# Kernel tuning notes

Measured on AMD Instinct MI355X. Metric: run time of the kernel, lower is better.

Reference implementation:

```python
import jax, jax.numpy as jnp
import numpy as np

B, IN, S, PD, P, D = 8192, 19000, 256, 128, 16, 64  # batch, input_dim, shared_dim, pathway_dim, n_pathways, n_drugs


def setup_inputs() -> dict:
    key = jax.random.key(0)
    ks = jax.random.split(key, 6)
    x = jax.random.normal(ks[0], (B, IN), dtype=jnp.float32)
    drug_indices = jax.random.randint(ks[1], (B,), 0, D, dtype=jnp.int32)
    W1 = jax.random.normal(ks[2], (IN, S), dtype=jnp.float32) / np.float32(np.sqrt(IN))
    b1 = jnp.zeros((S,), jnp.float32)
    Wp = jax.random.normal(ks[3], (P, S, PD), dtype=jnp.float32) / np.float32(np.sqrt(S))
    bp = jnp.zeros((P, PD), jnp.float32)
    Wd = jax.random.normal(ks[4], (D, PD), dtype=jnp.float32) / np.float32(np.sqrt(PD))
    bd = jnp.zeros((D,), jnp.float32)
    drug_to_pw = (jnp.arange(D, dtype=jnp.int32) % P)  # drug -> pathway routing table (i%16 per init_kwargs)
    return dict(x=x, drug_indices=drug_indices, W1=W1, b1=b1, Wp=Wp, bp=bp, Wd=Wd, bd=bd, drug_to_pw=drug_to_pw)


def reference(x, drug_indices, W1, b1, Wp, bp, Wd, bd, drug_to_pw):
    # shared encoder (dropout is identity in eval)
    h = jax.nn.relu(x @ W1 + b1)                                  # [B, S]
    # run all pathway experts densely (P is small), then per-sample select
    all_pw = jax.nn.relu(jnp.einsum('bs,psd->bpd', h, Wp) + bp)   # [B, P, PD]
    pw_idx = drug_to_pw[drug_indices]                             # [B]
    pw_out = jnp.take_along_axis(all_pw, pw_idx[:, None, None], axis=1)[:, 0]  # [B, PD]
    # per-sample drug head: gather row of Wd and dot
    out = jnp.sum(pw_out * Wd[drug_indices], axis=-1) + bd[drug_indices]       # [B]
    return out
```

## Files before the change

### kernel.cpp

```cpp
#include <hip/hip_runtime.h>

#define KREAL 19000
#define KP    19008
#define NSTEPS 594
#define BM 128
#define BN 256
#define MBLK 64
#define BATCH 8192
#define SDIM 256
#define PDIM 128

typedef __attribute__((ext_vector_type(8))) short frag_ab;
typedef __attribute__((ext_vector_type(4))) float frag_cd;

static __device__ __forceinline__ short f2bf(float f) {
    union { float f; unsigned u; } cv; cv.f = f;
    unsigned u = cv.u;
    u += 0x7fffu + ((u >> 16) & 1u);
    return (short)(u >> 16);
}

static __device__ __forceinline__ short4 cvt4(float4 v) {
    short4 p;
    p.x = f2bf(v.x); p.y = f2bf(v.y); p.z = f2bf(v.z); p.w = f2bf(v.w);
    return p;
}

__global__ void transpose_w1(const float* __restrict__ W1, short* __restrict__ W1t) {
    __shared__ float tile[32][33];
    int k0 = blockIdx.x * 32;
    int n0 = blockIdx.y * 32;
    int tx = threadIdx.x & 31;
    int ty = threadIdx.x >> 5;
#pragma unroll
    for (int i = 0; i < 32; i += 8) {
        int k = k0 + ty + i;
        tile[ty + i][tx] = (k < KREAL) ? W1[(long)k * SDIM + n0 + tx] : 0.f;
    }
    __syncthreads();
#pragma unroll
    for (int i = 0; i < 32; i += 8) {
        int n = n0 + ty + i;
        W1t[(long)n * KP + k0 + tx] = f2bf(tile[tx][ty + i]);
    }
}

__global__ __launch_bounds__(512, 2)
void gemm1(const float* __restrict__ x, const short* __restrict__ W1t,
           float* __restrict__ pout, int nch) {
    __shared__ short As[2][BM * 32];
    __shared__ short Bs[2][BN * 32];

    int bid = blockIdx.x;
    int mb, ch;
    if (nch == 4) {
        int xcd  = bid & 7;
        int slot = bid >> 3;
        ch = xcd >> 1;
        mb = ((xcd & 1) << 5) | slot;
    } else {
        mb = bid % MBLK;
        ch = bid / MBLK;
    }
    int m0 = mb * BM;
    int s0 = (NSTEPS * ch) / nch;
    int s1 = (NSTEPS * (ch + 1)) / nch;

    int tid  = threadIdx.x;
    int wave = tid >> 6;
    int lane = tid & 63;
    int wr = wave >> 2, wc = wave & 3;
    int lrow = lane & 15;
    int lq   = lane >> 4;

    int k4 = (tid & 7) << 2;
    const float* xp0 = x + (long)(m0 + (tid >> 3)) * KREAL + k4;
    const float* xp1 = xp0 + (long)64 * KREAL;
    const short* bp0 = W1t + (long)(tid >> 2) * KP + ((tid & 3) << 3);
    const short* bp1 = bp0 + (long)128 * KP;

    frag_cd acc[4][4];
#pragma unroll
    for (int i = 0; i < 4; i++)
#pragma unroll
        for (int j = 0; j < 4; j++) acc[i][j] = (frag_cd)(0.f);

    float4 ra0, ra1;
    int4   rb0, rb1;
    {
        int kb = s0 * 32;
        bool ok = (kb + k4 + 4 <= KREAL);
        ra0 = ok ? *(const float4*)(xp0 + kb) : make_float4(0.f, 0.f, 0.f, 0.f);
        ra1 = ok ? *(const float4*)(xp1 + kb) : make_float4(0.f, 0.f, 0.f, 0.f);
        rb0 = *(const int4*)(bp0 + kb);
        rb1 = *(const int4*)(bp1 + kb);
    }

    int buf = 0;
    for (int s = s0; s < s1; ++s) {
        *(short4*)(&As[buf][tid * 4])        = cvt4(ra0);
        *(short4*)(&As[buf][tid * 4 + 2048]) = cvt4(ra1);
        *(int4*)(&Bs[buf][tid * 8])          = rb0;
        *(int4*)(&Bs[buf][tid * 8 + 4096])   = rb1;
        if (s + 1 < s1) {
            int kb = (s + 1) * 32;
            bool ok = (kb + k4 + 4 <= KREAL);
            ra0 = ok ? *(const float4*)(xp0 + kb) : make_float4(0.f, 0.f, 0.f, 0.f);
            ra1 = ok ? *(const float4*)(xp1 + kb) : make_float4(0.f, 0.f, 0.f, 0.f);
            rb0 = *(const int4*)(bp0 + kb);
            rb1 = *(const int4*)(bp1 + kb);
        }
        __syncthreads();
        frag_ab af[4], bfr[4];
#pragma unroll
        for (int mt = 0; mt < 4; mt++)
            af[mt] = *(const frag_ab*)(&As[buf][(wr * 64 + mt * 16 + lrow) * 32 + lq * 8]);
#pragma unroll
        for (int nt = 0; nt < 4; nt++)
            bfr[nt] = *(const frag_ab*)(&Bs[buf][(wc * 64 + nt * 16 + lrow) * 32 + lq * 8]);
#pragma unroll
        for (int mt = 0; mt < 4; mt++)
#pragma unroll
            for (int nt = 0; nt < 4; nt++)
                acc[mt][nt] = __builtin_amdgcn_mfma_f32_16x16x32_bf16(
                    af[mt], bfr[nt], acc[mt][nt], 0, 0, 0);
        buf ^= 1;
    }

#pragma unroll
    for (int mt = 0; mt < 4; mt++)
#pragma unroll
        for (int nt = 0; nt < 4; nt++)
#pragma unroll
            for (int r = 0; r < 4; r++) {
                int row = m0 + wr * 64 + mt * 16 + lq * 4 + r;
                int col = wc * 64 + nt * 16 + lrow;
                pout[((long)ch * BATCH + row) * SDIM + col] = acc[mt][nt][r];
            }
}

__global__ void stage2(const float* __restrict__ pout, const float* __restrict__ b1,
                       const float* __restrict__ Wp, const float* __restrict__ bp,
                       const float* __restrict__ Wd, const float* __restrict__ bd,
                       const int* __restrict__ drug_idx, const int* __restrict__ d2p,
                       float* __restrict__ out, int nch) {
    __shared__ float h[SDIM];
    __shared__ float red[2];
    int b = blockIdx.x;
    int t = threadIdx.x;
    int drug = drug_idx[b];
    int p    = d2p[drug];

    for (int i = t; i < SDIM; i += 128) {
        float a = b1[i];
        for (int c = 0; c < nch; c++)
            a += pout[((long)c * BATCH + b) * SDIM + i];
        h[i] = fmaxf(a, 0.f);
    }
    __syncthreads();

    const float* wp = Wp + (long)p * SDIM * PDIM;
    float a = 0.f;
#pragma unroll 8
    for (int s = 0; s < SDIM; s++)
        a = fmaf(h[s], wp[s * PDIM + t], a);
    a += bp[p * PDIM + t];
    a = fmaxf(a, 0.f);

    float v = a * Wd[drug * PDIM + t];
#pragma unroll
    for (int off = 32; off; off >>= 1) v += __shfl_down(v, off, 64);
    if ((t & 63) == 0) red[t >> 6] = v;
    __syncthreads();
    if (t == 0) out[b] = red[0] + red[1] + bd[drug];
}

extern "C" void kernel_launch(void* const* d_in, const int* in_sizes, int n_in,
                              void* d_out, int out_size, void* d_ws, size_t ws_size,
                              hipStream_t stream) {
    const float* x    = (const float*)d_in[0];
    const int*   drug = (const int*)d_in[1];
    const float* W1   = (const float*)d_in[2];
    const float* b1   = (const float*)d_in[3];
    const float* Wp   = (const float*)d_in[4];
    const float* bp   = (const float*)d_in[5];
    const float* Wd   = (const float*)d_in[6];
    const float* bd   = (const float*)d_in[7];
    const int*   d2p  = (const int*)d_in[8];
    float* out = (float*)d_out;

    size_t pchunk    = (size_t)BATCH * SDIM * sizeof(float);
    size_t w1t_bytes = (size_t)SDIM * KP * sizeof(short);
    int nch = 4;
    if (ws_size < w1t_bytes + 4 * pchunk) {
        long avail = (long)ws_size - (long)w1t_bytes;
        nch = (int)(avail / (long)pchunk);
        if (nch < 1) nch = 1;
        if (nch > 4) nch = 4;
    }
    float* pout = (float*)d_ws;
    short* W1t  = (short*)((char*)d_ws + (size_t)nch * pchunk);

    hipLaunchKernelGGL(transpose_w1, dim3(NSTEPS, SDIM / 32), dim3(256), 0, stream,
                       W1, W1t);
    hipLaunchKernelGGL(gemm1, dim3(MBLK * nch), dim3(512), 0, stream,
                       x, W1t, pout, nch);
    hipLaunchKernelGGL(stage2, dim3(BATCH), dim3(128), 0, stream,
                       pout, b1, Wp, bp, Wd, bd, drug, d2p, out, nch);
}
```

Before: 910.4 us.

## Bucket samples by pathway so stage2 reuses expert weights across 32 samples

Adds a single-block bucketing kernel that groups batch indices by their routed pathway into 32-sample blocks. The pathway stage then processes each block together, loading each Wp column once and applying it to 32 cached hidden vectors in shared memory, instead of streaming the full 128 KB expert matrix once per sample. This cuts redundant Wp traffic in stage2, at the cost of an extra serial single-block launch and padded blocks.

After: 918.0 us. About the same (+0.8%).

```diff
diff --git a/kernel.cpp b/kernel.cpp
--- a/kernel.cpp
+++ b/kernel.cpp
@@ -9,6 +9,9 @@
 #define BATCH 8192
 #define SDIM 256
 #define PDIM 128
+#define NPW  16
+#define S2S  32
+#define MAXBLK 272
 
 typedef __attribute__((ext_vector_type(8))) short frag_ab;
 typedef __attribute__((ext_vector_type(4))) float frag_cd;
@@ -42,6 +45,49 @@
     for (int i = 0; i < 32; i += 8) {
         int n = n0 + ty + i;
         W1t[(long)n * KP + k0 + tx] = f2bf(tile[tx][ty + i]);
+    }
+}
+
+__global__ __launch_bounds__(1024)
+void bucket(const int* __restrict__ drug_idx, const int* __restrict__ d2p,
+            int* __restrict__ ord, int* __restrict__ blk_p) {
+    __shared__ int cnt[NPW];
+    __shared__ int pos[NPW];
+    __shared__ int pstart[NPW];
+    int t = threadIdx.x;
+    if (t < NPW) { cnt[t] = 0; pos[t] = 0; }
+    __syncthreads();
+
+    int myp[8];
+#pragma unroll
+    for (int r = 0; r < 8; r++) {
+        int i = t + r * 1024;
+        myp[r] = d2p[drug_idx[i]];
+        atomicAdd(&cnt[myp[r]], 1);
+    }
+    for (int i = t; i < MAXBLK * S2S; i += 1024) ord[i] = -1;
+    if (t < MAXBLK) blk_p[t] = -1;
+    __syncthreads();
+
+    if (t == 0) {
+        int bb = 0;
+        for (int p = 0; p < NPW; p++) {
+            pstart[p] = bb;
+            bb += (cnt[p] + S2S - 1) / S2S;
+        }
+    }
+    __syncthreads();
+
+    if (t < NPW) {
+        int p = t, nb = (cnt[p] + S2S - 1) / S2S, b0 = pstart[p];
+        for (int j = 0; j < nb; j++) blk_p[b0 + j] = p;
+    }
+#pragma unroll
+    for (int r = 0; r < 8; r++) {
+        int i = t + r * 1024;
+        int p = myp[r];
+        int j = atomicAdd(&pos[p], 1);
+        ord[pstart[p] * S2S + j] = i;
     }
 }
 
@@ -139,40 +185,84 @@
             }
 }
 
-__global__ void stage2(const float* __restrict__ pout, const float* __restrict__ b1,
-                       const float* __restrict__ Wp, const float* __restrict__ bp,
-                       const float* __restrict__ Wd, const float* __restrict__ bd,
-                       const int* __restrict__ drug_idx, const int* __restrict__ d2p,
-                       float* __restrict__ out, int nch) {
-    __shared__ float h[SDIM];
-    __shared__ float red[2];
-    int b = blockIdx.x;
+__global__ __launch_bounds__(256)
+void stage2(const float* __restrict__ pout, const float* __restrict__ b1,
+            const float* __restrict__ Wp, const float* __restrict__ bp,
+            const float* __restrict__ Wd, const float* __restrict__ bd,
+            const int* __restrict__ drug_idx,
+            const int* __restrict__ ord, const int* __restrict__ blk_p,
+            float* __restrict__ out, int nch) {
+    int g = blockIdx.x;
+    int p = blk_p[g];
+    if (p < 0) return;
+
+    __shared__ float hs[S2S][260];
+    __shared__ float pw[S2S][132];
+    __shared__ int   sidx[S2S];
+
     int t = threadIdx.x;
-    int drug = drug_idx[b];
-    int p    = d2p[drug];
-
-    for (int i = t; i < SDIM; i += 128) {
-        float a = b1[i];
-        for (int c = 0; c < nch; c++)
-            a += pout[((long)c * BATCH + b) * SDIM + i];
-        h[i] = fmaxf(a, 0.f);
-    }
-    __syncthreads();
-
-    const float* wp = Wp + (long)p * SDIM * PDIM;
-    float a = 0.f;
-#pragma unroll 8
-    for (int s = 0; s < SDIM; s++)
-        a = fmaf(h[s], wp[s * PDIM + t], a);
-    a += bp[p * PDIM + t];
-    a = fmaxf(a, 0.f);
-
-    float v = a * Wd[drug * PDIM + t];
-#pragma unroll
-    for (int off = 32; off; off >>= 1) v += __shfl_down(v, off, 64);
-    if ((t & 63) == 0) red[t >> 6] = v;
-    __syncthreads();
-    if (t == 0) out[b] = red[0] + red[1] + bd[drug];
+    if (t < S2S) sidx[t] = ord[g * S2S + t];
+    __syncthreads();
+
+    int si = t >> 3, l8 = t & 7;
+    int b = sidx[si];
+
+#pragma unroll
+    for (int v = 0; v < 8; v++) {
+        int i = (l8 + v * 8) * 4;
+        float4 a = *(const float4*)(b1 + i);
+        if (b >= 0) {
+            for (int c = 0; c < nch; c++) {
+                float4 q = *(const float4*)(pout + ((long)c * BATCH + b) * SDIM + i);
+                a.x += q.x; a.y += q.y; a.z += q.z; a.w += q.w;
+            }
+        }
+        float4 r;
+        r.x = fmaxf(a.x, 0.f); r.y = fmaxf(a.y, 0.f);
+        r.z = fmaxf(a.z, 0.f); r.w = fmaxf(a.w, 0.f);
+        *(float4*)(&hs[si][i]) = r;
+    }
+    __syncthreads();
+
+    int d = t & 127, half = t >> 7;
+    const float* wpc = Wp + (long)p * SDIM * PDIM + d;
+    float acc[16];
+#pragma unroll
+    for (int jj = 0; jj < 16; jj++) acc[jj] = 0.f;
+    for (int s4 = 0; s4 < SDIM; s4 += 4) {
+        float w0 = wpc[(s4 + 0) * PDIM];
+        float w1 = wpc[(s4 + 1) * PDIM];
+        float w2 = wpc[(s4 + 2) * PDIM];
+        float w3 = wpc[(s4 + 3) * PDIM];
+#pragma unroll
+        for (int jj = 0; jj < 16; jj++) {
+            float4 h4 = *(const float4*)(&hs[half * 16 + jj][s4]);
+            acc[jj] = fmaf(h4.x, w0, acc[jj]);
+            acc[jj] = fmaf(h4.y, w1, acc[jj]);
+            acc[jj] = fmaf(h4.z, w2, acc[jj]);
+            acc[jj] = fmaf(h4.w, w3, acc[jj]);
+        }
+    }
+    float bpv = bp[p * PDIM + d];
+#pragma unroll
+    for (int jj = 0; jj < 16; jj++)
+        pw[half * 16 + jj][d] = fmaxf(acc[jj] + bpv, 0.f);
+    __syncthreads();
+
+    if (b >= 0) {
+        int drug = drug_idx[b];
+        const float* wd = Wd + drug * PDIM;
+        float v = 0.f;
+#pragma unroll
+        for (int k = 0; k < 16; k++) {
+            int dd = l8 + k * 8;
+            v = fmaf(pw[si][dd], wd[dd], v);
+        }
+        v += __shfl_down(v, 4, 8);
+        v += __shfl_down(v, 2, 8);
+        v += __shfl_down(v, 1, 8);
+        if (l8 == 0) out[b] = v + bd[drug];
+    }
 }
 
 extern "C" void kernel_launch(void* const* d_in, const int* in_sizes, int n_in,
@@ -191,20 +281,26 @@
 
     size_t pchunk    = (size_t)BATCH * SDIM * sizeof(float);
     size_t w1t_bytes = (size_t)SDIM * KP * sizeof(short);
+    size_t ordb      = (size_t)MAXBLK * S2S * sizeof(int);
+    size_t blkb      = (size_t)MAXBLK * sizeof(int);
     int nch = 4;
-    if (ws_size < w1t_bytes + 4 * pchunk) {
-        long avail = (long)ws_size - (long)w1t_bytes;
+    if (ws_size < w1t_bytes + 4 * pchunk + ordb + blkb + 256) {
+        long avail = (long)ws_size - (long)(w1t_bytes + ordb + blkb + 256);
         nch = (int)(avail / (long)pchunk);
         if (nch < 1) nch = 1;
         if (nch > 4) nch = 4;
     }
-    float* pout = (float*)d_ws;
-    short* W1t  = (short*)((char*)d_ws + (size_t)nch * pchunk);
+    float* pout  = (float*)d_ws;
+    short* W1t   = (short*)((char*)d_ws + (size_t)nch * pchunk);
+    int*   ord   = (int*)((char*)d_ws + (size_t)nch * pchunk + w1t_bytes);
+    int*   blk_p = ord + MAXBLK * S2S;
 
     hipLaunchKernelGGL(transpose_w1, dim3(NSTEPS, SDIM / 32), dim3(256), 0, stream,
                        W1, W1t);
+    hipLaunchKernelGGL(bucket, dim3(1), dim3(1024), 0, stream,
+                       drug, d2p, ord, blk_p);
     hipLaunchKernelGGL(gemm1, dim3(MBLK * nch), dim3(512), 0, stream,
                        x, W1t, pout, nch);
-    hipLaunchKernelGGL(stage2, dim3(BATCH), dim3(128), 0, stream,
-                       pout, b1, Wp, bp, Wd, bd, drug, d2p, out, nch);
-}
+    hipLaunchKernelGGL(stage2, dim3(MAXBLK), dim3(256), 0, stream,
+                       pout, b1, Wp, bp, Wd, bd, drug, ord, blk_p, out, nch);
+}
```
